# Kernel tuning notes

Measured on AMD Instinct MI355X. Metric: run time of the kernel, lower is better.

The kernel has to match this reference:

```python
import jax, jax.numpy as jnp
import numpy as np

B, N, FIN, H, D = 4, 2048, 128, 4, 64
ALPHA = 0.2  # LeakyReLU negative slope


def _xavier_uniform(key, shape):
    fan_in, fan_out = shape[0], shape[1]
    limit = float(np.sqrt(6.0 / (fan_in + fan_out)))
    return jax.random.uniform(key, shape, jnp.float32, -limit, limit)


def setup_inputs() -> dict:
    key = jax.random.key(0)
    k1, k2, k3, k4 = jax.random.split(key, 4)
    x = jax.random.normal(k1, (B, N, FIN), jnp.float32)
    adj = jax.random.randint(k2, (B, N, N), 0, 2, jnp.int32)  # dense 0/1 mask
    W = _xavier_uniform(k3, (FIN, H * D))
    a = _xavier_uniform(k4, (2 * D, 1))
    return {"x": x, "adj": adj, "W": W, "a": a}


def reference(x, adj, W, a):
    Bb, Nn, _ = x.shape
    Dd = a.shape[0] // 2
    Hh = W.shape[1] // Dd
    # h: [B, N, H, D]
    h = (x @ W).reshape(Bb, Nn, Hh, Dd)
    # Additive attention: e[b,i,j,h] = leakyrelu(a1 . h[b,i,h] + a2 . h[b,j,h])
    a1 = a[:Dd, 0]
    a2 = a[Dd:, 0]
    ei = jnp.einsum('bnhd,d->bnh', h, a1)  # source (row i) term
    ej = jnp.einsum('bnhd,d->bnh', h, a2)  # dest (col j) term
    e = ei[:, :, None, :] + ej[:, None, :, :]  # [B, N, N, H]
    e = jnp.where(e >= 0, e, ALPHA * e)  # LeakyReLU
    e = jnp.where(adj[..., None] == 0, -jnp.inf, e)
    att = jax.nn.softmax(e, axis=2)  # softmax over neighbors j
    # dropout is a no-op in eval mode (training=False)
    out = jnp.einsum('bijh,bjhd->bihd', att, h)  # [B, N, H, D]
    return out.mean(axis=2)  # mean over heads -> [B, N, D]
```

## Files before the change

kernel.cpp:

```cpp
#include <hip/hip_runtime.h>

#define NN 2048
#define NH 4
#define DD 64
#define FIN 128
#define NB 4
#define LOG2E 1.44269504f

typedef unsigned short u16;
typedef unsigned int u32;
typedef short sh8 __attribute__((ext_vector_type(8)));
typedef float f32x4 __attribute__((ext_vector_type(4)));

static __device__ __forceinline__ u16 f2bf(float f) {
    u32 u = __builtin_bit_cast(u32, f);
    u += 0x7fffu + ((u >> 16) & 1u);
    return (u16)(u >> 16);
}
static __device__ __forceinline__ u32 pk_bf(float a, float b) {
    u32 ua = __builtin_bit_cast(u32, a) + 0x8000u;
    u32 ub = __builtin_bit_cast(u32, b) + 0x8000u;
    return __builtin_amdgcn_perm(ub, ua, 0x07060302u);
}
static __device__ __forceinline__ float fast_exp2(float x) {
    float r;
    asm("v_exp_f32 %0, %1" : "=v"(r) : "v"(x));
    return r;
}

static __device__ __forceinline__ void cd_probe(int ln15, int q, int* irow, int* icol) {
    sh8 pa, pb, qa, qb;
    #pragma unroll
    for (int ii = 0; ii < 8; ++ii) {
        pa[ii] = (short)f2bf((float)ln15);
        pb[ii] = 0;
        qa[ii] = 0;
        qb[ii] = (short)f2bf((float)ln15);
    }
    if (q == 0) { pb[0] = (short)f2bf(1.0f); qa[0] = (short)f2bf(1.0f); }
    f32x4 z = {};
    f32x4 prow = __builtin_amdgcn_mfma_f32_16x16x32_bf16(pa, pb, z, 0, 0, 0);
    f32x4 pcol = __builtin_amdgcn_mfma_f32_16x16x32_bf16(qa, qb, z, 0, 0, 0);
    #pragma unroll
    for (int r = 0; r < 4; ++r) {
        irow[r] = (int)(prow[r] + 0.5f);
        icol[r] = (int)(pcol[r] + 0.5f);
    }
}


__global__ __launch_bounds__(256)
void k_prep(const float* __restrict__ W, u16* __restrict__ WT) {
    const int bt  = blockIdx.x;
    const int kt  = bt & 3;
    const int ct8 = bt >> 2;
    __shared__ float tile[32][33];
    const int tid = threadIdx.x;
    const int rr = tid >> 5, cc = tid & 31;
    #pragma unroll
    for (int i = 0; i < 4; ++i)
        tile[rr + 8 * i][cc] = W[(size_t)(kt * 32 + rr + 8 * i) * 256 + ct8 * 32 + cc];
    __syncthreads();
    #pragma unroll
    for (int i = 0; i < 4; ++i)
        WT[(size_t)(ct8 * 32 + rr + 8 * i) * FIN + kt * 32 + cc] = f2bf(tile[cc][rr + 8 * i]);
}

__global__ __launch_bounds__(256)
void k_gemm_h(const float* __restrict__ x, const u16* __restrict__ WT,
              const float* __restrict__ a,
              u16* __restrict__ hTf, float* __restrict__ ei_g, float* __restrict__ ej_g) {
    const int nb = blockIdx.x, b = blockIdx.y;
    const int tid = threadIdx.x, hd = tid >> 6, lane = tid & 63, ln15 = lane & 15, q = lane >> 4;
    const int q8 = q * 8;
    const int n0 = nb * 64;

    __shared__ u16 xs[64][136];
    __shared__ float cs[NH][4][16][20];
    {
        const int col = (tid & 31) * 4;
        const int r0  = tid >> 5;
        #pragma unroll
        for (int rr = 0; rr < 8; ++rr) {
            const int row = r0 + rr * 8;
            const float4 v = *(const float4*)(x + ((size_t)(b * NN + n0 + row)) * FIN + col);
            *(u32*)&xs[row][col]     = pk_bf(v.x, v.y);
            *(u32*)&xs[row][col + 2] = pk_bf(v.z, v.w);
        }
    }
    __syncthreads();

    int irow[4], icol[4];
    cd_probe(ln15, q, irow, icol);

    f32x4 acc[4][4] = {};
    #pragma unroll
    for (int ks = 0; ks < 4; ++ks) {
        sh8 af[4], bfr[4];
        #pragma unroll
        for (int ct = 0; ct < 4; ++ct)
            af[ct] = *(const sh8*)(WT + (size_t)(hd * 64 + ct * 16 + ln15) * FIN + ks * 32 + q8);
        #pragma unroll
        for (int nt = 0; nt < 4; ++nt)
            bfr[nt] = *(const sh8*)&xs[nt * 16 + ln15][ks * 32 + q8];
        #pragma unroll
        for (int ct = 0; ct < 4; ++ct)
            #pragma unroll
            for (int nt = 0; nt < 4; ++nt)
                acc[ct][nt] = __builtin_amdgcn_mfma_f32_16x16x32_bf16(af[ct], bfr[nt], acc[ct][nt], 0, 0, 0);
    }

    float eip[4] = {}, ejq[4] = {};
    #pragma unroll
    for (int ct = 0; ct < 4; ++ct) {
        #pragma unroll
        for (int nt = 0; nt < 4; ++nt)
            #pragma unroll
            for (int r = 0; r < 4; ++r)
                cs[hd][nt][irow[r]][icol[r]] = acc[ct][nt][r];

        #pragma unroll
        for (int p = 0; p < 2; ++p) {
            const float4 c0 = *(const float4*)&cs[hd][2 * p + (q >> 1)][ln15][(q & 1) * 8];
            const float4 c1 = *(const float4*)&cs[hd][2 * p + (q >> 1)][ln15][(q & 1) * 8 + 4];
            uint4 o;
            o.x = pk_bf(c0.x, c0.y); o.y = pk_bf(c0.z, c0.w);
            o.z = pk_bf(c1.x, c1.y); o.w = pk_bf(c1.z, c1.w);
            *(uint4*)(hTf + ((((size_t)(b * NH + hd) * 64 + nb * 2 + p) * 4 + ct) * 512) + lane * 8) = o;
        }

        float a1v[4], a2v[4];
        #pragma unroll
        for (int r = 0; r < 4; ++r) {
            const int d = ct * 16 + 4 * q + r;
            a1v[r] = a[d] * LOG2E;
            a2v[r] = a[64 + d] * LOG2E;
        }
        #pragma unroll
        for (int nt = 0; nt < 4; ++nt)
            #pragma unroll
            for (int r = 0; r < 4; ++r) {
                const float v = cs[hd][nt][4 * q + r][ln15];
                eip[nt] += v * a1v[r];
                ejq[nt] += v * a2v[r];
            }
    }
    #pragma unroll
    for (int nt = 0; nt < 4; ++nt) {
        eip[nt] += __shfl_xor(eip[nt], 16);
        eip[nt] += __shfl_xor(eip[nt], 32);
        ejq[nt] += __shfl_xor(ejq[nt], 16);
        ejq[nt] += __shfl_xor(ejq[nt], 32);
    }
    if (lane < 16) {
        const size_t bhd = (size_t)(b * NH + hd) * NN;
        #pragma unroll
        for (int nt = 0; nt < 4; ++nt) {
            ei_g[bhd + n0 + nt * 16 + lane] = eip[nt];
            ej_g[bhd + n0 + nt * 16 + lane] = ejq[nt];
        }
    }
}

template <int NJT>
__global__ __launch_bounds__(256, 4)
void k_attn(const int* __restrict__ adj, const u16* __restrict__ hTf,
            const float* __restrict__ ei_g, const float* __restrict__ ej_g,
            float* __restrict__ o_part, float* __restrict__ l_part) {
    const int ib = blockIdx.x, js = blockIdx.y, b = blockIdx.z;
    const int js_n = gridDim.y;
    const int tid = threadIdx.x, hd = tid >> 6, lane = tid & 63, ln15 = lane & 15, q = lane >> 4;
    const int q8 = q * 8;
    const int iA = ib * 32 + ln15;
    const int jt0 = js * NJT;

    __shared__ u32 mlds[32][NJT + 1];
    __shared__ float ejs[NH][NJT * 32];

    {
        const int row = (hd << 3) + (lane >> 3);
        const int* abase = adj + (size_t)(b * NN + ib * 32 + row) * NN + jt0 * 32 + (lane & 7) * 4;
        #pragma unroll
        for (int jb = 0; jb < NJT; jb += 8) {
            int4 vv[8];
            #pragma unroll
            for (int u = 0; u < 8; ++u)
                vv[u] = *(const int4*)(abase + (jb + u) * 32);
            #pragma unroll
            for (int u = 0; u < 8; ++u) {
                u32 nib = (vv[u].x ? 1u : 0u) | (vv[u].y ? 2u : 0u) |
                          (vv[u].z ? 4u : 0u) | (vv[u].w ? 8u : 0u);
                u32 w = nib << (4 * (lane & 7));
                w |= __shfl_xor(w, 1);
                w |= __shfl_xor(w, 2);
                w |= __shfl_xor(w, 4);
                if ((lane & 7) == 0) mlds[row][jb + u] = w;
            }
        }
    }
    const size_t bhd = (size_t)(b * NH + hd) * NN;
    {
        const float* src = ej_g + bhd + jt0 * 32;
        #pragma unroll
        for (int u = 0; u < NJT / 8; ++u) {
            const int o4 = (u * 64 + lane) * 4;
            *(float4*)&ejs[hd][o4] = *(const float4*)(src + o4);
        }
    }
    __syncthreads();

    int irow[4], icol[4];
    cd_probe(ln15, q, irow, icol);

    const float eivA = ei_g[bhd + iA];
    const float eivB = ei_g[bhd + iA + 16];
    const u16*  hfp  = hTf + (size_t)(b * NH + hd) * (64 * 2048) + (size_t)lane * 8;

    sh8 ones;
    #pragma unroll
    for (int ii = 0; ii < 8; ++ii) ones[ii] = (short)0x3F80;

    f32x4 acc[8] = {};
    f32x4 accl[2] = {};

    sh8 H[2][4];
    #pragma unroll
    for (int s = 0; s < 2; ++s)
        #pragma unroll
        for (int k = 0; k < 4; ++k)
            H[s][k] = *(const sh8*)(hfp + (size_t)(jt0 + s) * 2048 + k * 512);

    #pragma unroll
    for (int t = 0; t < NJT; ++t) {
        const u32 mA = mlds[ln15][t];
        const u32 mB = mlds[ln15 + 16][t];
        const float4 e0 = *(const float4*)&ejs[hd][t * 32 + q8];
        const float4 e1 = *(const float4*)&ejs[hd][t * 32 + q8 + 4];

        const float ef[8] = { e0.x, e0.y, e0.z, e0.w, e1.x, e1.y, e1.z, e1.w };
        const u32 mqA = mA >> q8;
        const u32 mqB = mB >> q8;
        float pA[8], pB[8];
        #pragma unroll
        for (int ii = 0; ii < 8; ++ii) {
            float eA = eivA + ef[ii];
            float eB = eivB + ef[ii];
            eA = fmaxf(eA, 0.2f * eA);
            eB = fmaxf(eB, 0.2f * eB);
            const float xA = fast_exp2(eA);
            const float xB = fast_exp2(eB);
            pA[ii] = (mqA & (1u << ii)) ? xA : 0.f;
            pB[ii] = (mqB & (1u << ii)) ? xB : 0.f;
        }
        union { uint4 u; sh8 v; } avA, avB;
        avA.u.x = pk_bf(pA[0], pA[1]); avA.u.y = pk_bf(pA[2], pA[3]);
        avA.u.z = pk_bf(pA[4], pA[5]); avA.u.w = pk_bf(pA[6], pA[7]);
        avB.u.x = pk_bf(pB[0], pB[1]); avB.u.y = pk_bf(pB[2], pB[3]);
        avB.u.z = pk_bf(pB[4], pB[5]); avB.u.w = pk_bf(pB[6], pB[7]);

        acc[0] = __builtin_amdgcn_mfma_f32_16x16x32_bf16(avA.v, H[t & 1][0], acc[0], 0, 0, 0);
        acc[1] = __builtin_amdgcn_mfma_f32_16x16x32_bf16(avA.v, H[t & 1][1], acc[1], 0, 0, 0);
        acc[2] = __builtin_amdgcn_mfma_f32_16x16x32_bf16(avA.v, H[t & 1][2], acc[2], 0, 0, 0);
        acc[3] = __builtin_amdgcn_mfma_f32_16x16x32_bf16(avA.v, H[t & 1][3], acc[3], 0, 0, 0);
        accl[0] = __builtin_amdgcn_mfma_f32_16x16x32_bf16(avA.v, ones, accl[0], 0, 0, 0);
        acc[4] = __builtin_amdgcn_mfma_f32_16x16x32_bf16(avB.v, H[t & 1][0], acc[4], 0, 0, 0);
        acc[5] = __builtin_amdgcn_mfma_f32_16x16x32_bf16(avB.v, H[t & 1][1], acc[5], 0, 0, 0);
        acc[6] = __builtin_amdgcn_mfma_f32_16x16x32_bf16(avB.v, H[t & 1][2], acc[6], 0, 0, 0);
        acc[7] = __builtin_amdgcn_mfma_f32_16x16x32_bf16(avB.v, H[t & 1][3], acc[7], 0, 0, 0);
        accl[1] = __builtin_amdgcn_mfma_f32_16x16x32_bf16(avB.v, ones, accl[1], 0, 0, 0);

        if (t + 2 < NJT) {
            #pragma unroll
            for (int k = 0; k < 4; ++k)
                H[t & 1][k] = *(const sh8*)(hfp + (size_t)(jt0 + t + 2) * 2048 + k * 512);
        }
    }

    const size_t pbA = (((size_t)b * 128 + ib * 2 + 0) * js_n + js) * NH + hd;
    const size_t pbB = (((size_t)b * 128 + ib * 2 + 1) * js_n + js) * NH + hd;
    #pragma unroll
    for (int r = 0; r < 4; ++r) {
        l_part[pbA * 16 + irow[r]] = accl[0][r];
        l_part[pbB * 16 + irow[r]] = accl[1][r];
    }
    float* opA = o_part + pbA * 1024;
    float* opB = o_part + pbB * 1024;
    #pragma unroll
    for (int dt = 0; dt < 4; ++dt)
        #pragma unroll
        for (int r = 0; r < 4; ++r) {
            opA[(size_t)irow[r] * 64 + dt * 16 + icol[r]] = acc[dt][r];
            opB[(size_t)irow[r] * 64 + dt * 16 + icol[r]] = acc[4 + dt][r];
        }
}

template <int JS>
__global__ __launch_bounds__(256)
void k_combine(const float* __restrict__ o_part, const float* __restrict__ l_part,
               float* __restrict__ out) {
    const int ib = blockIdx.x, b = blockIdx.y;
    const int tid = threadIdx.x;
    const int i = tid >> 4, d4 = (tid & 15) * 4;
    float4 sacc = {0.f, 0.f, 0.f, 0.f};
    #pragma unroll
    for (int h = 0; h < NH; ++h) {
        float l = 0.f;
        float4 oh = {0.f, 0.f, 0.f, 0.f};
        #pragma unroll
        for (int js = 0; js < JS; ++js) {
            const size_t pbase = (((size_t)b * 128 + ib) * JS + js) * NH + h;
            l += l_part[pbase * 16 + i];
            const float4 ov = *(const float4*)(o_part + pbase * 1024 + (size_t)i * 64 + d4);
            oh.x += ov.x; oh.y += ov.y; oh.z += ov.z; oh.w += ov.w;
        }
        const float inv = 0.25f / l;
        sacc.x += oh.x * inv; sacc.y += oh.y * inv;
        sacc.z += oh.z * inv; sacc.w += oh.w * inv;
    }
    *(float4*)(out + ((size_t)(b * NN) + ib * 16 + i) * DD + d4) = sacc;
}

extern "C" void kernel_launch(void* const* d_in, const int* in_sizes, int n_in,
                              void* d_out, int out_size, void* d_ws, size_t ws_size,
                              hipStream_t stream) {
    const float* x = nullptr; const int* adj = nullptr;
    const float* W = nullptr; const float* a = nullptr;
    for (int i = 0; i < n_in; ++i) {
        switch (in_sizes[i]) {
            case NB * NN * FIN:  x   = (const float*)d_in[i]; break;
            case NB * NN * NN:   adj = (const int*)d_in[i];   break;
            case FIN * 256:      W   = (const float*)d_in[i]; break;
            case 2 * DD:         a   = (const float*)d_in[i]; break;
            default: break;
        }
    }
    if (!x)   x   = (const float*)d_in[0];
    if (!adj) adj = (const int*)d_in[1];
    if (!W)   W   = (const float*)d_in[2];
    if (!a)   a   = (const float*)d_in[3];
    float* out = (float*)d_out;

    char* ws = (char*)d_ws;
    u16*   WT  = (u16*)(ws);
    float* ei  = (float*)(ws + 65536);
    float* ej  = (float*)(ws + 196608);
    u16*   hTf = (u16*)(ws + 327680);
    float* l_p = (float*)(ws + 6619136);
    float* o_p = (float*)(ws + 7143424);

    const size_t need4 = 7143424 + (size_t)4 * 8388608;
    const size_t need2 = 7143424 + (size_t)2 * 8388608;
    const int js_n = (ws_size >= need4) ? 4 : (ws_size >= need2) ? 2 : 1;

    k_prep<<<dim3(32), dim3(256), 0, stream>>>(W, WT);
    k_gemm_h<<<dim3(32, NB), dim3(256), 0, stream>>>(x, WT, a, hTf, ei, ej);
    if (js_n == 4)
        k_attn<16><<<dim3(64, 4, NB), dim3(256), 0, stream>>>(adj, hTf, ei, ej, o_p, l_p);
    else if (js_n == 2)
        k_attn<32><<<dim3(64, 2, NB), dim3(256), 0, stream>>>(adj, hTf, ei, ej, o_p, l_p);
    else
        k_attn<64><<<dim3(64, 1, NB), dim3(256), 0, stream>>>(adj, hTf, ei, ej, o_p, l_p);
    if (js_n == 4)      k_combine<4><<<dim3(128, NB), dim3(256), 0, stream>>>(o_p, l_p, out);
    else if (js_n == 2) k_combine<2><<<dim3(128, NB), dim3(256), 0, stream>>>(o_p, l_p, out);
    else                k_combine<1><<<dim3(128, NB), dim3(256), 0, stream>>>(o_p, l_p, out);
}
```

Before: 136.9 us.

## Double attention block rows to 64 so two waves share H tiles

```diff
diff --git a/kernel.cpp b/kernel.cpp
--- a/kernel.cpp
+++ b/kernel.cpp
@@ -163,23 +163,26 @@
 }
 
 template <int NJT>
-__global__ __launch_bounds__(256, 4)
+__global__ __launch_bounds__(512, 4)
 void k_attn(const int* __restrict__ adj, const u16* __restrict__ hTf,
             const float* __restrict__ ei_g, const float* __restrict__ ej_g,
             float* __restrict__ o_part, float* __restrict__ l_part) {
     const int ib = blockIdx.x, js = blockIdx.y, b = blockIdx.z;
     const int js_n = gridDim.y;
-    const int tid = threadIdx.x, hd = tid >> 6, lane = tid & 63, ln15 = lane & 15, q = lane >> 4;
+    const int tid = threadIdx.x;
+    const int w = tid >> 6;
+    const int hd = w & 3, ihalf = w >> 2;
+    const int lane = tid & 63, ln15 = lane & 15, q = lane >> 4;
     const int q8 = q * 8;
-    const int iA = ib * 32 + ln15;
+    const int iA = ib * 64 + ihalf * 32 + ln15;
     const int jt0 = js * NJT;
 
-    __shared__ u32 mlds[32][NJT + 1];
+    __shared__ u32 mlds[64][NJT + 1];
     __shared__ float ejs[NH][NJT * 32];
 
     {
-        const int row = (hd << 3) + (lane >> 3);
-        const int* abase = adj + (size_t)(b * NN + ib * 32 + row) * NN + jt0 * 32 + (lane & 7) * 4;
+        const int row = (w << 3) + (lane >> 3);
+        const int* abase = adj + (size_t)(b * NN + ib * 64 + row) * NN + jt0 * 32 + (lane & 7) * 4;
         #pragma unroll
         for (int jb = 0; jb < NJT; jb += 8) {
             int4 vv[8];
@@ -190,11 +193,11 @@
             for (int u = 0; u < 8; ++u) {
                 u32 nib = (vv[u].x ? 1u : 0u) | (vv[u].y ? 2u : 0u) |
                           (vv[u].z ? 4u : 0u) | (vv[u].w ? 8u : 0u);
-                u32 w = nib << (4 * (lane & 7));
-                w |= __shfl_xor(w, 1);
-                w |= __shfl_xor(w, 2);
-                w |= __shfl_xor(w, 4);
-                if ((lane & 7) == 0) mlds[row][jb + u] = w;
+                u32 wd = nib << (4 * (lane & 7));
+                wd |= __shfl_xor(wd, 1);
+                wd |= __shfl_xor(wd, 2);
+                wd |= __shfl_xor(wd, 4);
+                if ((lane & 7) == 0) mlds[row][jb + u] = wd;
             }
         }
     }
@@ -202,7 +205,7 @@
     {
         const float* src = ej_g + bhd + jt0 * 32;
         #pragma unroll
-        for (int u = 0; u < NJT / 8; ++u) {
+        for (int u = ihalf; u < NJT / 8; u += 2) {
             const int o4 = (u * 64 + lane) * 4;
             *(float4*)&ejs[hd][o4] = *(const float4*)(src + o4);
         }
@@ -230,10 +233,12 @@
         for (int k = 0; k < 4; ++k)
             H[s][k] = *(const sh8*)(hfp + (size_t)(jt0 + s) * 2048 + k * 512);
 
+    const int mrow = ihalf * 32 + ln15;
+
     #pragma unroll
     for (int t = 0; t < NJT; ++t) {
-        const u32 mA = mlds[ln15][t];
-        const u32 mB = mlds[ln15 + 16][t];
+        const u32 mA = mlds[mrow][t];
+        const u32 mB = mlds[mrow + 16][t];
         const float4 e0 = *(const float4*)&ejs[hd][t * 32 + q8];
         const float4 e1 = *(const float4*)&ejs[hd][t * 32 + q8 + 4];
 
@@ -276,8 +281,9 @@
         }
     }
 
-    const size_t pbA = (((size_t)b * 128 + ib * 2 + 0) * js_n + js) * NH + hd;
-    const size_t pbB = (((size_t)b * 128 + ib * 2 + 1) * js_n + js) * NH + hd;
+    const int i16 = ib * 4 + ihalf * 2;
+    const size_t pbA = (((size_t)b * 128 + i16 + 0) * js_n + js) * NH + hd;
+    const size_t pbB = (((size_t)b * 128 + i16 + 1) * js_n + js) * NH + hd;
     #pragma unroll
     for (int r = 0; r < 4; ++r) {
         l_part[pbA * 16 + irow[r]] = accl[0][r];
@@ -355,11 +361,11 @@
     k_prep<<<dim3(32), dim3(256), 0, stream>>>(W, WT);
     k_gemm_h<<<dim3(32, NB), dim3(256), 0, stream>>>(x, WT, a, hTf, ei, ej);
     if (js_n == 4)
-        k_attn<16><<<dim3(64, 4, NB), dim3(256), 0, stream>>>(adj, hTf, ei, ej, o_p, l_p);
+        k_attn<16><<<dim3(32, 4, NB), dim3(512), 0, stream>>>(adj, hTf, ei, ej, o_p, l_p);
     else if (js_n == 2)
-        k_attn<32><<<dim3(64, 2, NB), dim3(256), 0, stream>>>(adj, hTf, ei, ej, o_p, l_p);
+        k_attn<32><<<dim3(32, 2, NB), dim3(512), 0, stream>>>(adj, hTf, ei, ej, o_p, l_p);
     else
-        k_attn<64><<<dim3(64, 1, NB), dim3(256), 0, stream>>>(adj, hTf, ei, ej, o_p, l_p);
+        k_attn<64><<<dim3(32, 1, NB), dim3(512), 0, stream>>>(adj, hTf, ei, ej, o_p, l_p);
     if (js_n == 4)      k_combine<4><<<dim3(128, NB), dim3(256), 0, stream>>>(o_p, l_p, out);
     else if (js_n == 2) k_combine<2><<<dim3(128, NB), dim3(256), 0, stream>>>(o_p, l_p, out);
     else                k_combine<1><<<dim3(128, NB), dim3(256), 0, stream>>>(o_p, l_p, out);
```

Measured after the change: 136.1 us. Within noise of the previous version (-0.6%).
